# Optimization experiments

Hardware: AMD Instinct MI355X
Metric: run time of the kernel (lower is better)

Reference implementation:

```python
import jax, jax.numpy as jnp
import numpy as np

B, T, E, D = 4, 1024, 1024, 2048   # batch, dec len, enc len, model dim
N, K, H = 16, 8, 256               # q heads, kv heads, head dim
G = N // K                         # GQA group size
SCALE = H ** -0.5                  # query_pre_attn_scalar
SOFT_CAP = 50.0
EPS = 1e-6
ROPE_BASE = 10000.0
_K_MASK = jnp.finfo(jnp.bfloat16).min


def _rms_norm(x, scale, eps=EPS):
    var = jnp.mean(jnp.square(x), axis=-1, keepdims=True)
    return x * jax.lax.rsqrt(var + eps) * (1.0 + scale)


def _apply_rope(x, positions, base=ROPE_BASE):
    # x: [B, L, n, H], positions: [B, L]; rope_proportion=1.0, scale_factor=1.0
    h = x.shape[-1]
    freq_exp = 2.0 / h * jnp.arange(h // 2, dtype=jnp.float32)
    timescale = base ** freq_exp                                  # [H/2]
    ang = (positions.astype(jnp.float32)[..., None] / timescale)[..., None, :]  # [B,L,1,H/2]
    sin, cos = jnp.sin(ang), jnp.cos(ang)
    x1, x2 = jnp.split(x, 2, axis=-1)
    out = jnp.concatenate([x1 * cos - x2 * sin, x2 * cos + x1 * sin], axis=-1)
    return out.astype(x.dtype)


def setup_inputs() -> dict:
    key = jax.random.key(0)
    ks = jax.random.split(key, 8)
    hidden_states = jax.random.normal(ks[0], (B, T, D), jnp.float32)
    encoder_hidden_states = jax.random.normal(ks[1], (B, E, D), jnp.float32)
    position_ids = jnp.broadcast_to(jnp.arange(T, dtype=jnp.int32)[None, :], (B, T))
    # merged mask: causal over self part, full visibility over cross part
    causal = jnp.tril(jnp.ones((T, T), jnp.bool_))
    cross = jnp.ones((T, E), jnp.bool_)
    merged_attention_mask = jnp.broadcast_to(
        jnp.concatenate([causal, cross], axis=-1)[None, None], (B, 1, T, T + E))
    w = 0.02
    q_w = jax.random.normal(ks[2], (N, D, H), jnp.float32) * w
    k_w = jax.random.normal(ks[3], (K, D, H), jnp.float32) * w
    v_w = jax.random.normal(ks[4], (K, D, H), jnp.float32) * w
    o_w = jax.random.normal(ks[5], (N, H, D), jnp.float32) * w
    q_scale = jax.random.normal(ks[6], (H,), jnp.float32) * w
    k_scale = jax.random.normal(ks[7], (H,), jnp.float32) * w
    return dict(hidden_states=hidden_states, encoder_hidden_states=encoder_hidden_states,
                position_ids=position_ids, merged_attention_mask=merged_attention_mask,
                q_w=q_w, k_w=k_w, v_w=v_w, o_w=o_w, q_scale=q_scale, k_scale=k_scale)


def reference(hidden_states, encoder_hidden_states, position_ids, merged_attention_mask,
              q_w, k_w, v_w, o_w, q_scale, k_scale):
    # QKV projections
    query = jnp.einsum('BTD,NDH->BTNH', hidden_states, q_w)
    self_key = jnp.einsum('BTD,KDH->BTKH', hidden_states, k_w)
    self_value = jnp.einsum('BTD,KDH->BTKH', hidden_states, v_w)
    # QK-RMSNorm
    query = _rms_norm(query, q_scale)
    self_key = _rms_norm(self_key, k_scale)
    # RoPE on self-attention q/k only
    query = _apply_rope(query, position_ids)
    self_key = _apply_rope(self_key, position_ids)
    # Cross K/V from encoder states (no RoPE)
    cross_key = _rms_norm(jnp.einsum('BTD,KDH->BTKH', encoder_hidden_states, k_w), k_scale)
    cross_value = jnp.einsum('BTD,KDH->BTKH', encoder_hidden_states, v_w)
    # Merge self + cross along key axis
    keys = jnp.concatenate([self_key, cross_key], axis=1)       # [B, T+E, K, H]
    values = jnp.concatenate([self_value, cross_value], axis=1)
    # Scaled GQA attention
    q = (query * SCALE).reshape(B, T, K, G, H)
    logits = jnp.einsum('BTKGH,BSKH->BKGTS', q, keys)
    # logit soft-capping
    logits = SOFT_CAP * jnp.tanh(logits / SOFT_CAP)
    mask = merged_attention_mask[:, :, None]                    # [B,1,1,T,S]
    logits = jnp.where(mask, logits, _K_MASK)
    probs = jax.nn.softmax(logits.astype(jnp.float32), axis=-1).astype(keys.dtype)
    attn = jnp.einsum('BKGTS,BSKH->BTKGH', probs, values).reshape(B, T, N, H)
    return jnp.einsum('BTNH,NHD->BTD', attn, o_w)
```

## Files before the change

kernel.cpp:

```cpp
#include <hip/hip_runtime.h>
#include <hip/hip_bf16.h>
#include <cstdio>


typedef __attribute__((ext_vector_type(8))) short bf16x8;
typedef __attribute__((ext_vector_type(4))) float f32x4;

static __device__ __forceinline__ ushort f2bf(float x){
  uint u = __float_as_uint(x);
  u += 0x7fffu + ((u >> 16) & 1u);
  return (ushort)(u >> 16);
}
static __device__ __forceinline__ float bf2f(ushort u){
  return __uint_as_float((uint)u << 16);
}

__global__ void k_detect(const uint* __restrict__ src, int* __restrict__ flag){
  int lane = threadIdx.x & 63;
  int cnt = 0;
  for (int i = 0; i < 4; i++){
    uint w = src[lane * 4 + i];
    uint e = (w >> 7) & 0xffu;
    cnt += (e >= 90u && e <= 141u) ? 1 : 0;
  }
  for (int o = 1; o < 64; o <<= 1) cnt += __shfl_xor(cnt, o);
  if (lane == 0) *flag = (cnt >= 128) ? 1 : 0;
}

__global__ void k_tobf(const void* __restrict__ src, ushort* __restrict__ dst,
                       int n8, const int* __restrict__ flag){
  int i = blockIdx.x * blockDim.x + threadIdx.x;
  if (i >= n8) return;
  if (*flag){
    reinterpret_cast<uint4*>(dst)[i] = reinterpret_cast<const uint4*>(src)[i];
  } else {
    const float4* s = reinterpret_cast<const float4*>(src);
    float4 a = s[i * 2], b = s[i * 2 + 1];
    ushort o[8] = { f2bf(a.x), f2bf(a.y), f2bf(a.z), f2bf(a.w),
                    f2bf(b.x), f2bf(b.y), f2bf(b.z), f2bf(b.w) };
    reinterpret_cast<uint4*>(dst)[i] = *reinterpret_cast<uint4*>(o);
  }
}

__global__ void k_wtrans(const ushort* __restrict__ in, ushort* __restrict__ out, int R, int C){
  __shared__ ushort t[32][33];
  int p = blockIdx.z;
  int r0 = blockIdx.y * 32, c0 = blockIdx.x * 32;
  const ushort* ip = in + (size_t)p * R * C;
  ushort* op = out + (size_t)p * R * C;
  int cc = threadIdx.x & 31, rr = threadIdx.x >> 5;
  for (int i = 0; i < 32; i += 8)
    t[rr + i][cc] = ip[(size_t)(r0 + rr + i) * C + c0 + cc];
  __syncthreads();
  for (int i = 0; i < 32; i += 8)
    op[(size_t)(c0 + rr + i) * R + r0 + cc] = t[cc][rr + i];
}

template<int EPI, typename OutT>
__global__ __launch_bounds__(256)
void k_gemm_bt(const ushort* __restrict__ A0, const ushort* __restrict__ A1, int Msplit,
               const ushort* __restrict__ Bm, OutT* __restrict__ Cout,
               int M, int N, int Kd){
  constexpr int STR = 40;
  __shared__ ushort As[128 * STR];
  __shared__ ushort Bs[128 * STR];
  const int tid = threadIdx.x;
  const int m0 = blockIdx.y * 128, n0 = blockIdx.x * 128;
  const ushort* Ap = (m0 < Msplit) ? (A0 + (size_t)m0 * Kd)
                                   : (A1 + (size_t)(m0 - Msplit) * Kd);
  const ushort* Bp = Bm + (size_t)n0 * Kd;
  const int w = tid >> 6, lane = tid & 63, c = lane & 15, q = lane >> 4;
  const int wr = (w >> 1) * 64, wc = (w & 1) * 64;

  f32x4 zf = {0.f, 0.f, 0.f, 0.f};
  f32x4 acc[4][4];
  for (int mi = 0; mi < 4; mi++) for (int ni = 0; ni < 4; ni++) acc[mi][ni] = zf;

  const int sr = tid >> 2, sc8 = (tid & 3) * 8;
  for (int k0 = 0; k0 < Kd; k0 += 32){
    for (int i = 0; i < 2; i++){
      int r = sr + i * 64;
      *reinterpret_cast<uint4*>(&As[r * STR + sc8]) =
        *reinterpret_cast<const uint4*>(Ap + (size_t)r * Kd + k0 + sc8);
      *reinterpret_cast<uint4*>(&Bs[r * STR + sc8]) =
        *reinterpret_cast<const uint4*>(Bp + (size_t)r * Kd + k0 + sc8);
    }
    __syncthreads();
    bf16x8 af[4], bfrg[4];
    for (int mi = 0; mi < 4; mi++)
      af[mi] = *reinterpret_cast<const bf16x8*>(&As[(wr + mi * 16 + c) * STR + q * 8]);
    for (int ni = 0; ni < 4; ni++)
      bfrg[ni] = *reinterpret_cast<const bf16x8*>(&Bs[(wc + ni * 16 + c) * STR + q * 8]);
    for (int mi = 0; mi < 4; mi++)
      for (int ni = 0; ni < 4; ni++)
        acc[mi][ni] = __builtin_amdgcn_mfma_f32_16x16x32_bf16(af[mi], bfrg[ni], acc[mi][ni], 0, 0, 0);
    __syncthreads();
  }

  for (int mi = 0; mi < 4; mi++)
    for (int ni = 0; ni < 4; ni++){
      int gr0 = m0 + wr + mi * 16 + q * 4;
      int gc  = n0 + wc + ni * 16 + c;
      if constexpr (EPI == 0){
        for (int r = 0; r < 4; r++){
          if constexpr (sizeof(OutT) == 2)
            Cout[(size_t)(gr0 + r) * N + gc] = (OutT)f2bf(acc[mi][ni][r]);
          else
            Cout[(size_t)(gr0 + r) * N + gc] = (OutT)acc[mi][ni][r];
        }
      } else if constexpr (EPI == 1){
        for (int r = 0; r < 4; r++){
          int gr = gr0 + r, b, s;
          if (gr < 4096){ b = gr >> 10; s = gr & 1023; }
          else { int g2 = gr - 4096; b = g2 >> 10; s = 1024 + (g2 & 1023); }
          Cout[(size_t)(b * 2048 + s) * N + gc] = (OutT)f2bf(acc[mi][ni][r]);
        }
      } else {
        int gr = gr0, b, s;
        if (gr < 4096){ b = gr >> 10; s = gr & 1023; }
        else { int g2 = gr - 4096; b = g2 >> 10; s = 1024 + (g2 & 1023); }
        int kk = gc >> 8, h = gc & 255;
        ushort4 o;
        o.x = f2bf(acc[mi][ni][0]); o.y = f2bf(acc[mi][ni][1]);
        o.z = f2bf(acc[mi][ni][2]); o.w = f2bf(acc[mi][ni][3]);
        *reinterpret_cast<ushort4*>((ushort*)Cout + ((size_t)(b * 8 + kk) * 256 + h) * 2048 + s) = o;
      }
    }
}

__global__ __launch_bounds__(256)
void k_norm_q(const ushort* __restrict__ Qraw, const int* __restrict__ pos,
              const ushort* __restrict__ scale, ushort* __restrict__ Qbf){
  int w = threadIdx.x >> 6, lane = threadIdx.x & 63;
  int gw = blockIdx.x * 4 + w;
  int bt = gw >> 4;
  ushort4 xu = *reinterpret_cast<const ushort4*>(Qraw + (size_t)gw * 256 + lane * 4);
  float x[4] = { bf2f(xu.x), bf2f(xu.y), bf2f(xu.z), bf2f(xu.w) };
  float ss = x[0]*x[0] + x[1]*x[1] + x[2]*x[2] + x[3]*x[3];
  for (int o = 32; o > 0; o >>= 1) ss += __shfl_xor(ss, o);
  float rin = rsqrtf(ss * (1.f / 256.f) + 1e-6f);
  ushort4 su = *reinterpret_cast<const ushort4*>(scale + lane * 4);
  float y[4] = { x[0] * rin * (1.f + bf2f(su.x)), x[1] * rin * (1.f + bf2f(su.y)),
                 x[2] * rin * (1.f + bf2f(su.z)), x[3] * rin * (1.f + bf2f(su.w)) };
  float oth[4];
  for (int i = 0; i < 4; i++) oth[i] = __shfl_xor(y[i], 32);
  bool hi = lane >= 32;
  float fb = (float)((lane & 31) * 4);
  float p = (float)pos[bt];
  ushort4 o;
  ushort* op[4] = {&o.x, &o.y, &o.z, &o.w};
  for (int i = 0; i < 4; i++){
    float fi = fb + i;
    float tsi = expf(fi * -0.07195578415f);
    float ang = p * tsi;
    float sn, cs; sincosf(ang, &sn, &cs);
    float v = hi ? (y[i] * cs + oth[i] * sn) : (y[i] * cs - oth[i] * sn);
    *op[i] = f2bf(v * 0.0625f);
  }
  *reinterpret_cast<ushort4*>(Qbf + (size_t)gw * 256 + lane * 4) = o;
}

__global__ __launch_bounds__(256)
void k_norm_k(const ushort* __restrict__ Kraw, const int* __restrict__ pos,
              const ushort* __restrict__ scale, ushort* __restrict__ Kbf){
  int w = threadIdx.x >> 6, lane = threadIdx.x & 63;
  int gw = blockIdx.x * 4 + w;
  int row = gw >> 3;
  int s = row & 2047, b = row >> 11;
  ushort4 xu = *reinterpret_cast<const ushort4*>(Kraw + (size_t)gw * 256 + lane * 4);
  float x[4] = { bf2f(xu.x), bf2f(xu.y), bf2f(xu.z), bf2f(xu.w) };
  float ss = x[0]*x[0] + x[1]*x[1] + x[2]*x[2] + x[3]*x[3];
  for (int o = 32; o > 0; o >>= 1) ss += __shfl_xor(ss, o);
  float rin = rsqrtf(ss * (1.f / 256.f) + 1e-6f);
  ushort4 su = *reinterpret_cast<const ushort4*>(scale + lane * 4);
  float y[4] = { x[0] * rin * (1.f + bf2f(su.x)), x[1] * rin * (1.f + bf2f(su.y)),
                 x[2] * rin * (1.f + bf2f(su.z)), x[3] * rin * (1.f + bf2f(su.w)) };
  ushort4 o;
  ushort* op[4] = {&o.x, &o.y, &o.z, &o.w};
  if (s < 1024){
    float oth[4];
    for (int i = 0; i < 4; i++) oth[i] = __shfl_xor(y[i], 32);
    bool hi = lane >= 32;
    float fb = (float)((lane & 31) * 4);
    float p = (float)pos[b * 1024 + s];
    for (int i = 0; i < 4; i++){
      float fi = fb + i;
      float tsi = expf(fi * -0.07195578415f);
      float ang = p * tsi;
      float sn, cs; sincosf(ang, &sn, &cs);
      float v = hi ? (y[i] * cs + oth[i] * sn) : (y[i] * cs - oth[i] * sn);
      *op[i] = f2bf(v);
    }
  } else {
    for (int i = 0; i < 4; i++) *op[i] = f2bf(y[i]);
  }
  *reinterpret_cast<ushort4*>(Kbf + (size_t)gw * 256 + lane * 4) = o;
}

__global__ __launch_bounds__(256)
void k_attn(const ushort* __restrict__ Qbf, const ushort* __restrict__ Kbf,
            const ushort* __restrict__ Vt, ushort* __restrict__ attn){
  constexpr int KSs = 264, VSs = 40, PSs = 40;
  __shared__ ushort Ks[32 * KSs];
  __shared__ ushort Vs[256 * VSs];
  __shared__ ushort Pm[4][16 * PSs];
  int b = blockIdx.z, n = blockIdx.y, t0 = blockIdx.x * 64;
  int kk = n >> 1;
  int tid = threadIdx.x, w = tid >> 6, lane = tid & 63, c = lane & 15, q = lane >> 4;

  bf16x8 qf[8];
  {
    int tq = t0 + w * 16 + c;
    const ushort* qp = Qbf + ((size_t)(b * 1024 + tq) * 16 + n) * 256 + q * 8;
    for (int f = 0; f < 8; f++) qf[f] = *reinterpret_cast<const bf16x8*>(qp + f * 32);
  }
  f32x4 zf = {0.f, 0.f, 0.f, 0.f};
  f32x4 accO[16];
  for (int i = 0; i < 16; i++) accO[i] = zf;
  float lacc[4] = {0.f, 0.f, 0.f, 0.f};

  const ushort* Kbase = Kbf + ((size_t)b * 2048 * 8 + kk) * 256;
  const ushort* Vbase = Vt + (size_t)(b * 8 + kk) * 256 * 2048;
  int nself = (t0 >> 5) + 2;
  int ntile = nself + 32;
  for (int it = 0; it < ntile; ++it){
    int s0 = (it < nself) ? it * 32 : 1024 + (it - nself) * 32;
    for (int i = 0; i < 4; i++){
      int tau = tid + i * 256;
      int r = tau >> 5, ch = (tau & 31) * 8;
      *reinterpret_cast<uint4*>(&Ks[r * KSs + ch]) =
        *reinterpret_cast<const uint4*>(Kbase + (size_t)(s0 + r) * 2048 + ch);
    }
    for (int i = 0; i < 4; i++){
      int tau = tid + i * 256;
      int h = tau >> 2, ch = (tau & 3) * 8;
      *reinterpret_cast<uint4*>(&Vs[h * VSs + ch]) =
        *reinterpret_cast<const uint4*>(Vbase + (size_t)h * 2048 + s0 + ch);
    }
    __syncthreads();
    f32x4 accL[2]; accL[0] = zf; accL[1] = zf;
    for (int ni = 0; ni < 2; ni++)
      for (int f = 0; f < 8; f++){
        bf16x8 kb = *reinterpret_cast<const bf16x8*>(&Ks[(ni * 16 + c) * KSs + f * 32 + q * 8]);
        accL[ni] = __builtin_amdgcn_mfma_f32_16x16x32_bf16(qf[f], kb, accL[ni], 0, 0, 0);
      }
    ushort* pw = Pm[w];
    for (int ni = 0; ni < 2; ni++)
      for (int r = 0; r < 4; r++){
        int s = s0 + ni * 16 + c;
        int t = t0 + w * 16 + q * 4 + r;
        float x = accL[ni][r] * 0.02f;
        float xc = fminf(fmaxf(x, -10.f), 10.f);
        float e2 = __expf(2.f * xc);
        float l2 = 50.f * (1.f - 2.f / (e2 + 1.f));
        float pv = (s >= 1024 || s <= t) ? __expf(l2) : 0.f;
        lacc[r] += pv;
        pw[(q * 4 + r) * PSs + ni * 16 + c] = f2bf(pv);
      }
    __asm__ volatile("s_waitcnt lgkmcnt(0)" ::: "memory");
    bf16x8 pa = *reinterpret_cast<const bf16x8*>(&pw[c * PSs + q * 8]);
    for (int hi = 0; hi < 16; hi++){
      bf16x8 vb = *reinterpret_cast<const bf16x8*>(&Vs[(hi * 16 + c) * VSs + q * 8]);
      accO[hi] = __builtin_amdgcn_mfma_f32_16x16x32_bf16(pa, vb, accO[hi], 0, 0, 0);
    }
    __syncthreads();
  }
  for (int r = 0; r < 4; r++)
    for (int o = 1; o < 16; o <<= 1) lacc[r] += __shfl_xor(lacc[r], o);
  float inv[4];
  for (int r = 0; r < 4; r++) inv[r] = 1.f / fmaxf(lacc[r], 1e-37f);
  for (int hi = 0; hi < 16; hi++)
    for (int r = 0; r < 4; r++){
      int t = t0 + w * 16 + q * 4 + r;
      attn[((size_t)(b * 1024 + t) * 16 + n) * 256 + hi * 16 + c] = f2bf(accO[hi][r] * inv[r]);
    }
}

extern "C" void kernel_launch(void* const* d_in, const int* in_sizes, int n_in,
                              void* d_out, int out_size, void* d_ws, size_t ws_size,
                              hipStream_t stream){
  const void* hidden = d_in[0];
  const void* enc    = d_in[1];
  const int*  posids = (const int*)d_in[2];
  const void* qw = d_in[4];
  const void* kw = d_in[5];
  const void* vw = d_in[6];
  const void* ow = d_in[7];
  const void* qs = d_in[8];
  const void* ks = d_in[9];
  float* out = (float*)d_out;

  char* ws = (char*)d_ws;
  size_t off = 0;
  auto alloc = [&](size_t sz){ void* p = ws + off; off += sz; return p; };
  ushort* Hb  = (ushort*)alloc(16777216);
  ushort* Eb  = (ushort*)alloc(16777216);
  ushort* Wq = (ushort*)alloc(16777216);
  ushort* Wk = (ushort*)alloc(8388608);
  ushort* Wv = (ushort*)alloc(8388608);
  ushort* Wo = (ushort*)alloc(16777216);
  ushort* Qbf = (ushort*)alloc(33554432);
  ushort* Kbf = (ushort*)alloc(33554432);
  char* S1 = (char*)alloc(67108864);
  ushort* qsb = (ushort*)alloc(512);
  ushort* ksb = (ushort*)alloc(512);
  int* flag  = (int*)alloc(64);
  ushort* qwc = (ushort*)S1;
  ushort* kwc = (ushort*)(S1 + 16777216);
  ushort* vwc = (ushort*)(S1 + 25165824);
  ushort* owc = (ushort*)(S1 + 33554432);
  ushort* Qraw = (ushort*)S1;
  ushort* Kraw = (ushort*)S1;
  ushort* Vt   = (ushort*)S1;
  ushort* attnb = (ushort*)(S1 + 33554432);
  if (off > ws_size){
    fprintf(stderr, "kernel_launch: ws too small: need %zu, have %zu\n", off, ws_size);
    return;
  }

  k_detect<<<1, 64, 0, stream>>>((const uint*)hidden, flag);
  k_tobf<<<4096, 256, 0, stream>>>(hidden, Hb, 1048576, flag);
  k_tobf<<<4096, 256, 0, stream>>>(enc,    Eb, 1048576, flag);
  k_tobf<<<4096, 256, 0, stream>>>(qw, qwc, 1048576, flag);
  k_tobf<<<2048, 256, 0, stream>>>(kw, kwc,  524288, flag);
  k_tobf<<<2048, 256, 0, stream>>>(vw, vwc,  524288, flag);
  k_tobf<<<4096, 256, 0, stream>>>(ow, owc, 1048576, flag);
  k_tobf<<<1, 256, 0, stream>>>(qs, qsb, 32, flag);
  k_tobf<<<1, 256, 0, stream>>>(ks, ksb, 32, flag);

  k_wtrans<<<dim3(8, 64, 16), 256, 0, stream>>>(qwc, Wq, 2048, 256);
  k_wtrans<<<dim3(8, 64, 8),  256, 0, stream>>>(kwc, Wk, 2048, 256);
  k_wtrans<<<dim3(8, 64, 8),  256, 0, stream>>>(vwc, Wv, 2048, 256);
  k_wtrans<<<dim3(64, 128, 1), 256, 0, stream>>>(owc, Wo, 4096, 2048);

  k_gemm_bt<0, ushort><<<dim3(32, 32), 256, 0, stream>>>(Hb, Hb, 1 << 30, Wq, Qraw, 4096, 4096, 2048);
  k_norm_q<<<16384, 256, 0, stream>>>(Qraw, posids, qsb, Qbf);
  k_gemm_bt<1, ushort><<<dim3(16, 64), 256, 0, stream>>>(Hb, Eb, 4096, Wk, Kraw, 8192, 2048, 2048);
  k_norm_k<<<16384, 256, 0, stream>>>(Kraw, posids, ksb, Kbf);
  k_gemm_bt<2, ushort><<<dim3(16, 64), 256, 0, stream>>>(Hb, Eb, 4096, Wv, Vt, 8192, 2048, 2048);

  k_attn<<<dim3(16, 16, 4), 256, 0, stream>>>(Qbf, Kbf, Vt, attnb);

  k_gemm_bt<0, float><<<dim3(16, 32), 256, 0, stream>>>(attnb, attnb, 1 << 30, Wo, out, 4096, 2048, 4096);
}
```

Measured before the change: 1.015 ms.

## Fuse weight cast into transpose, use direct-to-LDS loads, remap attention blocks per XCD

Three independent changes. The weight transpose kernel now reads fp32 or bf16 directly and converts while transposing, so the separate conversion passes and their intermediate buffers are gone. The GEMM stages A/B tiles with global_load_lds straight into LDS and drops row padding, which may bring back LDS bank conflicts on fragment reads. The attention grid becomes 1D with a swizzle that keeps each batch/kv-head group on one XCD so the shared K/V stays in that XCD's L2.

```diff
diff --git a/kernel.cpp b/kernel.cpp
--- a/kernel.cpp
+++ b/kernel.cpp
@@ -14,6 +14,10 @@
 static __device__ __forceinline__ float bf2f(ushort u){
   return __uint_as_float((uint)u << 16);
 }
+#define GLL16(gp, lp)                                                          \
+  __builtin_amdgcn_global_load_lds(                                            \
+      (const __attribute__((address_space(1))) void*)(gp),                     \
+      (__attribute__((address_space(3))) void*)(lp), 16, 0, 0)
 
 __global__ void k_detect(const uint* __restrict__ src, int* __restrict__ flag){
   int lane = threadIdx.x & 63;
@@ -42,15 +46,23 @@
   }
 }
 
-__global__ void k_wtrans(const ushort* __restrict__ in, ushort* __restrict__ out, int R, int C){
+__global__ void k_wtrans(const void* __restrict__ in, ushort* __restrict__ out,
+                         int R, int C, const int* __restrict__ flag){
   __shared__ ushort t[32][33];
+  int isbf = *flag;
   int p = blockIdx.z;
   int r0 = blockIdx.y * 32, c0 = blockIdx.x * 32;
-  const ushort* ip = in + (size_t)p * R * C;
   ushort* op = out + (size_t)p * R * C;
   int cc = threadIdx.x & 31, rr = threadIdx.x >> 5;
-  for (int i = 0; i < 32; i += 8)
-    t[rr + i][cc] = ip[(size_t)(r0 + rr + i) * C + c0 + cc];
+  if (isbf){
+    const ushort* ip = (const ushort*)in + (size_t)p * R * C;
+    for (int i = 0; i < 32; i += 8)
+      t[rr + i][cc] = ip[(size_t)(r0 + rr + i) * C + c0 + cc];
+  } else {
+    const float* ip = (const float*)in + (size_t)p * R * C;
+    for (int i = 0; i < 32; i += 8)
+      t[rr + i][cc] = f2bf(ip[(size_t)(r0 + rr + i) * C + c0 + cc]);
+  }
   __syncthreads();
   for (int i = 0; i < 32; i += 8)
     op[(size_t)(c0 + rr + i) * R + r0 + cc] = t[cc][rr + i];
@@ -61,9 +73,8 @@
 void k_gemm_bt(const ushort* __restrict__ A0, const ushort* __restrict__ A1, int Msplit,
                const ushort* __restrict__ Bm, OutT* __restrict__ Cout,
                int M, int N, int Kd){
-  constexpr int STR = 40;
-  __shared__ ushort As[128 * STR];
-  __shared__ ushort Bs[128 * STR];
+  __shared__ ushort As[128 * 32];
+  __shared__ ushort Bs[128 * 32];
   const int tid = threadIdx.x;
   const int m0 = blockIdx.y * 128, n0 = blockIdx.x * 128;
   const ushort* Ap = (m0 < Msplit) ? (A0 + (size_t)m0 * Kd)
@@ -77,20 +88,23 @@
   for (int mi = 0; mi < 4; mi++) for (int ni = 0; ni < 4; ni++) acc[mi][ni] = zf;
 
   const int sr = tid >> 2, sc8 = (tid & 3) * 8;
+  const ushort* ga = Ap + (size_t)sr * Kd + sc8;
+  const ushort* gb = Bp + (size_t)sr * Kd + sc8;
+  ushort* la = &As[sr * 32 + sc8];
+  ushort* lb = &Bs[sr * 32 + sc8];
+  const size_t rowskip = (size_t)64 * Kd;
+
   for (int k0 = 0; k0 < Kd; k0 += 32){
-    for (int i = 0; i < 2; i++){
-      int r = sr + i * 64;
-      *reinterpret_cast<uint4*>(&As[r * STR + sc8]) =
-        *reinterpret_cast<const uint4*>(Ap + (size_t)r * Kd + k0 + sc8);
-      *reinterpret_cast<uint4*>(&Bs[r * STR + sc8]) =
-        *reinterpret_cast<const uint4*>(Bp + (size_t)r * Kd + k0 + sc8);
-    }
+    GLL16(ga + k0,           la);
+    GLL16(ga + k0 + rowskip, la + 64 * 32);
+    GLL16(gb + k0,           lb);
+    GLL16(gb + k0 + rowskip, lb + 64 * 32);
     __syncthreads();
     bf16x8 af[4], bfrg[4];
     for (int mi = 0; mi < 4; mi++)
-      af[mi] = *reinterpret_cast<const bf16x8*>(&As[(wr + mi * 16 + c) * STR + q * 8]);
+      af[mi] = *reinterpret_cast<const bf16x8*>(&As[(wr + mi * 16 + c) * 32 + q * 8]);
     for (int ni = 0; ni < 4; ni++)
-      bfrg[ni] = *reinterpret_cast<const bf16x8*>(&Bs[(wc + ni * 16 + c) * STR + q * 8]);
+      bfrg[ni] = *reinterpret_cast<const bf16x8*>(&Bs[(wc + ni * 16 + c) * 32 + q * 8]);
     for (int mi = 0; mi < 4; mi++)
       for (int ni = 0; ni < 4; ni++)
         acc[mi][ni] = __builtin_amdgcn_mfma_f32_16x16x32_bf16(af[mi], bfrg[ni], acc[mi][ni], 0, 0, 0);
@@ -204,8 +218,13 @@
   __shared__ ushort Ks[32 * KSs];
   __shared__ ushort Vs[256 * VSs];
   __shared__ ushort Pm[4][16 * PSs];
-  int b = blockIdx.z, n = blockIdx.y, t0 = blockIdx.x * 64;
-  int kk = n >> 1;
+  int id = blockIdx.x;
+  int xcd = id & 7, slot = id >> 3;
+  int grp = xcd + 8 * (slot >> 5);
+  int within = slot & 31;
+  int b = grp >> 3, kk = grp & 7;
+  int n = kk * 2 + (within >> 4);
+  int t0 = (within & 15) * 64;
   int tid = threadIdx.x, w = tid >> 6, lane = tid & 63, c = lane & 15, q = lane >> 4;
 
   bf16x8 qf[8];
@@ -305,10 +324,6 @@
   ushort* qsb = (ushort*)alloc(512);
   ushort* ksb = (ushort*)alloc(512);
   int* flag  = (int*)alloc(64);
-  ushort* qwc = (ushort*)S1;
-  ushort* kwc = (ushort*)(S1 + 16777216);
-  ushort* vwc = (ushort*)(S1 + 25165824);
-  ushort* owc = (ushort*)(S1 + 33554432);
   ushort* Qraw = (ushort*)S1;
   ushort* Kraw = (ushort*)S1;
   ushort* Vt   = (ushort*)S1;
@@ -321,17 +336,13 @@
   k_detect<<<1, 64, 0, stream>>>((const uint*)hidden, flag);
   k_tobf<<<4096, 256, 0, stream>>>(hidden, Hb, 1048576, flag);
   k_tobf<<<4096, 256, 0, stream>>>(enc,    Eb, 1048576, flag);
-  k_tobf<<<4096, 256, 0, stream>>>(qw, qwc, 1048576, flag);
-  k_tobf<<<2048, 256, 0, stream>>>(kw, kwc,  524288, flag);
-  k_tobf<<<2048, 256, 0, stream>>>(vw, vwc,  524288, flag);
-  k_tobf<<<4096, 256, 0, stream>>>(ow, owc, 1048576, flag);
   k_tobf<<<1, 256, 0, stream>>>(qs, qsb, 32, flag);
   k_tobf<<<1, 256, 0, stream>>>(ks, ksb, 32, flag);
 
-  k_wtrans<<<dim3(8, 64, 16), 256, 0, stream>>>(qwc, Wq, 2048, 256);
-  k_wtrans<<<dim3(8, 64, 8),  256, 0, stream>>>(kwc, Wk, 2048, 256);
-  k_wtrans<<<dim3(8, 64, 8),  256, 0, stream>>>(vwc, Wv, 2048, 256);
-  k_wtrans<<<dim3(64, 128, 1), 256, 0, stream>>>(owc, Wo, 4096, 2048);
+  k_wtrans<<<dim3(8, 64, 16), 256, 0, stream>>>(qw, Wq, 2048, 256, flag);
+  k_wtrans<<<dim3(8, 64, 8),  256, 0, stream>>>(kw, Wk, 2048, 256, flag);
+  k_wtrans<<<dim3(8, 64, 8),  256, 0, stream>>>(vw, Wv, 2048, 256, flag);
+  k_wtrans<<<dim3(64, 128, 1), 256, 0, stream>>>(ow, Wo, 4096, 2048, flag);
 
   k_gemm_bt<0, ushort><<<dim3(32, 32), 256, 0, stream>>>(Hb, Hb, 1 << 30, Wq, Qraw, 4096, 4096, 2048);
   k_norm_q<<<16384, 256, 0, stream>>>(Qraw, posids, qsb, Qbf);
@@ -339,7 +350,7 @@
   k_norm_k<<<16384, 256, 0, stream>>>(Kraw, posids, ksb, Kbf);
   k_gemm_bt<2, ushort><<<dim3(16, 64), 256, 0, stream>>>(Hb, Eb, 4096, Wv, Vt, 8192, 2048, 2048);
 
-  k_attn<<<dim3(16, 16, 4), 256, 0, stream>>>(Qbf, Kbf, Vt, attnb);
+  k_attn<<<1024, 256, 0, stream>>>(Qbf, Kbf, Vt, attnb);
 
   k_gemm_bt<0, float><<<dim3(16, 32), 256, 0, stream>>>(attnb, attnb, 1 << 30, Wo, out, 4096, 2048, 4096);
 }
```

Measured after the change: 960.0 us. 1.06x faster.
